# Kernel optimization log

Hardware: AMD Instinct MI355X
Metric: run time of the kernel (lower is better)

Reference implementation:

```python
import jax, jax.numpy as jnp
import numpy as np

B, S, D, H = 2, 2048, 1024, 16
DK = D // H  # 64
ROPE_THETA = 10000.0


def apply_rope(t, positions):
    # t: [B, H, S, DK]; positions: [B, S]
    half = DK // 2
    inv_freq = 1.0 / (ROPE_THETA ** (jnp.arange(0, DK, 2, dtype=jnp.float32) / DK))  # [half]
    ang = positions.astype(jnp.float32)[:, None, :, None] * inv_freq  # [B,1,S,half]
    cos, sin = jnp.cos(ang), jnp.sin(ang)
    t_even = t[..., 0::2]
    t_odd = t[..., 1::2]
    r_even = t_even * cos - t_odd * sin
    r_odd = t_even * sin + t_odd * cos
    # interleave back to original layout
    return jnp.stack([r_even, r_odd], axis=-1).reshape(t.shape)


def setup_inputs() -> dict:
    key = jax.random.key(0)
    ks = jax.random.split(key, 5)
    x = jax.random.normal(ks[0], (B, S, D), dtype=jnp.float32)
    token_positions = jnp.broadcast_to(jnp.arange(S, dtype=jnp.int64 if jax.config.jax_enable_x64 else jnp.int32), (B, S))
    w_q = jax.random.normal(ks[1], (D, D), dtype=jnp.float32)
    w_k = jax.random.normal(ks[2], (D, D), dtype=jnp.float32)
    w_v = jax.random.normal(ks[3], (D, D), dtype=jnp.float32)
    w_o = jax.random.normal(ks[4], (D, D), dtype=jnp.float32)
    return {"x": x, "token_positions": token_positions, "w_q": w_q, "w_k": w_k, "w_v": w_v, "w_o": w_o}


def reference(x, token_positions, w_q, w_k, w_v, w_o):
    # project: weights stored as (h*d_k, d_model)
    wq = w_q.reshape(H, DK, D)
    wk = w_k.reshape(H, DK, D)
    wv = w_v.reshape(H, DK, D)
    q = jnp.einsum('bsd,hkd->bhsk', x, wq)  # [B,H,S,DK]
    k = jnp.einsum('bsd,hkd->bhsk', x, wk)
    v = jnp.einsum('bsd,hkd->bhsk', x, wv)
    q = apply_rope(q, token_positions)
    k = apply_rope(k, token_positions)
    scale = 1.0 / jnp.sqrt(jnp.float32(DK))
    scores = jnp.einsum('bhnk,bhmk->bhnm', q, k) * scale  # [B,H,S,S]
    causal = jnp.tril(jnp.ones((S, S), dtype=bool))
    scores = jnp.where(causal, scores, -jnp.inf)
    attn = jax.nn.softmax(scores, axis=-1)
    out = jnp.einsum('bhnm,bhmv->bhnv', attn, v)  # [B,H,S,DK]
    out = jnp.transpose(out, (0, 2, 1, 3)).reshape(B, S, H * DK)
    return jnp.einsum('bsf,df->bsd', out, w_o)
```

## Files before the change

### kernel.cpp

```cpp
#include <hip/hip_runtime.h>

typedef unsigned short u16;
typedef unsigned int u32;
typedef __attribute__((ext_vector_type(8))) __bf16 bf16x8;
typedef __attribute__((ext_vector_type(4))) float f32x4;

#define NSEQ 2048
#define NDIM 1024
#define NHEAD 16
#define NTOK 4096
#define NX   4194304
#define NWEL 1048576

__device__ __forceinline__ u16 f2bf(float f) {
  unsigned u = __float_as_uint(f);
  return (u16)((u + 0x7fffu + ((u >> 16) & 1u)) >> 16);
}
__device__ __forceinline__ float bf2f(u16 h) {
  return __uint_as_float(((unsigned)h) << 16);
}
__device__ __forceinline__ bf16x8 ld16(const u16* p) {
  int4 v = *reinterpret_cast<const int4*>(p);
  return __builtin_bit_cast(bf16x8, v);
}
__device__ __forceinline__ f32x4 mfma16(bf16x8 a, bf16x8 b, f32x4 c) {
  return __builtin_amdgcn_mfma_f32_16x16x32_bf16(a, b, c, 0, 0, 0);
}
__device__ __forceinline__ u32 cvtpk(float lo, float hi) {
  u32 r;
  asm("v_cvt_pk_bf16_f32 %0, %1, %2" : "=v"(r) : "v"(lo), "v"(hi));
  return r;
}
__device__ __forceinline__ float max3f(float a, float b, float c) {
  float d;
  asm("v_max3_f32 %0, %1, %2, %3" : "=v"(d) : "v"(a), "v"(b), "v"(c));
  return d;
}
__device__ __forceinline__ void gload16(const u16* g, u16* l) {
  __builtin_amdgcn_global_load_lds(
      (const __attribute__((address_space(1))) void*)g,
      (__attribute__((address_space(3))) void*)l, 16, 0, 0);
}

#define GEMM_PROLOGUE                                                         \
  const int tid = threadIdx.x;                                                \
  const int lane = tid & 63, wid = tid >> 6;                                  \
  const int wm = wid >> 1, wn = wid & 1;                                      \
  const int lr = lane & 15, lg = lane >> 4;                                   \
  const int srow_ = tid >> 2;                                                 \
  const int sch_ = ((tid & 3) ^ ((tid >> 3) & 3)) * 8;                        \
  const int rsw_ = (lg ^ ((lr >> 1) & 3)) * 8;

#define STAGE3(BB, AH, AL, BH, BL, T0, J0, K0)                                \
  {                                                                           \
    u16* bb_ = (BB);                                                          \
    gload16(AH + (size_t)((T0) + srow_) * NDIM + (K0) + sch_, bb_ + tid * 8); \
    gload16(AH + (size_t)((T0) + 64 + srow_) * NDIM + (K0) + sch_,            \
            bb_ + 2048 + tid * 8);                                            \
    gload16(BH + (size_t)((J0) + srow_) * NDIM + (K0) + sch_,                 \
            bb_ + 4096 + tid * 8);                                            \
    gload16(BH + (size_t)((J0) + 64 + srow_) * NDIM + (K0) + sch_,            \
            bb_ + 6144 + tid * 8);                                            \
    gload16(AL + (size_t)((T0) + srow_) * NDIM + (K0) + sch_,                 \
            bb_ + 8192 + tid * 8);                                            \
    gload16(AL + (size_t)((T0) + 64 + srow_) * NDIM + (K0) + sch_,            \
            bb_ + 10240 + tid * 8);                                           \
    gload16(BL + (size_t)((J0) + srow_) * NDIM + (K0) + sch_,                 \
            bb_ + 12288 + tid * 8);                                           \
    gload16(BL + (size_t)((J0) + 64 + srow_) * NDIM + (K0) + sch_,            \
            bb_ + 14336 + tid * 8);                                           \
  }

#define GEMM3_LOOP(AH, AL, BH, BL, T0, J0)                                    \
  STAGE3(lds, AH, AL, BH, BL, T0, J0, 0)                                      \
  __syncthreads();                                                            \
  for (int k0 = 0; k0 < NDIM; k0 += 32) {                                     \
    u16* cb_ = lds + ((k0 >> 5) & 1) * 16384;                                 \
    if (k0 + 32 < NDIM) {                                                     \
      u16* nb_ = lds + ((((k0 >> 5) & 1) ^ 1) * 16384);                       \
      STAGE3(nb_, AH, AL, BH, BL, T0, J0, k0 + 32)                            \
    }                                                                         \
    bf16x8 afh[4], afl[4];                                                    \
    _Pragma("unroll") for (int m = 0; m < 4; m++) {                           \
      int off = (wm * 64 + m * 16 + lr) * 32 + rsw_;                          \
      afh[m] = ld16(cb_ + off);                                               \
      afl[m] = ld16(cb_ + 8192 + off);                                        \
    }                                                                         \
    _Pragma("unroll") for (int n = 0; n < 4; n++) {                           \
      int off = (wn * 64 + n * 16 + lr) * 32 + rsw_;                          \
      bf16x8 bfh = ld16(cb_ + 4096 + off);                                    \
      bf16x8 bfl = ld16(cb_ + 12288 + off);                                   \
      _Pragma("unroll") for (int m = 0; m < 4; m++) {                         \
        acc[m][n] = mfma16(afh[m], bfh, acc[m][n]);                           \
        acc[m][n] = mfma16(afh[m], bfl, acc[m][n]);                           \
        acc[m][n] = mfma16(afl[m], bfh, acc[m][n]);                           \
      }                                                                       \
    }                                                                         \
    __syncthreads();                                                          \
  }

#define STAGE1(BB, AH, BH, T0, J0, K0)                                        \
  {                                                                           \
    u16* bb_ = (BB);                                                          \
    gload16(AH + (size_t)((T0) + srow_) * NDIM + (K0) + sch_, bb_ + tid * 8); \
    gload16(AH + (size_t)((T0) + 64 + srow_) * NDIM + (K0) + sch_,            \
            bb_ + 2048 + tid * 8);                                            \
    gload16(BH + (size_t)((J0) + srow_) * NDIM + (K0) + sch_,                 \
            bb_ + 4096 + tid * 8);                                            \
    gload16(BH + (size_t)((J0) + 64 + srow_) * NDIM + (K0) + sch_,            \
            bb_ + 6144 + tid * 8);                                            \
  }

#define GEMM1_LOOP(AH, BH, T0, J0)                                            \
  STAGE1(lds, AH, BH, T0, J0, 0)                                              \
  __syncthreads();                                                            \
  for (int k0 = 0; k0 < NDIM; k0 += 32) {                                     \
    u16* cb_ = lds + ((k0 >> 5) & 1) * 8192;                                  \
    if (k0 + 32 < NDIM) {                                                     \
      u16* nb_ = lds + ((((k0 >> 5) & 1) ^ 1) * 8192);                        \
      STAGE1(nb_, AH, BH, T0, J0, k0 + 32)                                    \
    }                                                                         \
    bf16x8 afh[4];                                                            \
    _Pragma("unroll") for (int m = 0; m < 4; m++) {                           \
      int off = (wm * 64 + m * 16 + lr) * 32 + rsw_;                          \
      afh[m] = ld16(cb_ + off);                                               \
    }                                                                         \
    _Pragma("unroll") for (int n = 0; n < 4; n++) {                           \
      int off = (wn * 64 + n * 16 + lr) * 32 + rsw_;                          \
      bf16x8 bfh = ld16(cb_ + 4096 + off);                                    \
      _Pragma("unroll") for (int m = 0; m < 4; m++) {                         \
        acc[m][n] = mfma16(afh[m], bfh, acc[m][n]);                           \
      }                                                                       \
    }                                                                         \
    __syncthreads();                                                          \
  }

__global__ __launch_bounds__(256) void k_prep(
    const float* __restrict__ x, const float* __restrict__ wq,
    const float* __restrict__ wk, const float* __restrict__ wv,
    const float* __restrict__ wo,
    u16* __restrict__ xh, u16* __restrict__ xl,
    u16* __restrict__ wh, u16* __restrict__ wl) {
  int g = blockIdx.x * 256 + threadIdx.x;
  const float4* src;
  u16 *dh, *dl;
  int idx;
  bool wantlo = true;
  if (g < NX / 4) {
    src = (const float4*)x; dh = xh; dl = xl; idx = g;
  } else {
    int z = (g - NX / 4) / (NWEL / 4);
    int r = (g - NX / 4) % (NWEL / 4);
    src = (const float4*)(z == 0 ? wq : z == 1 ? wk : z == 2 ? wv : wo);
    dh = wh + (size_t)z * NWEL; dl = wl + (size_t)z * NWEL; idx = r;
    wantlo = (z < 2);
  }
  float4 v = src[idx];
  u16 h0 = f2bf(v.x), h1 = f2bf(v.y), h2 = f2bf(v.z), h3 = f2bf(v.w);
  ushort4 hv = make_ushort4(h0, h1, h2, h3);
  ((ushort4*)dh)[idx] = hv;
  if (wantlo) {
    ushort4 lv = make_ushort4(f2bf(v.x - bf2f(h0)), f2bf(v.y - bf2f(h1)),
                              f2bf(v.z - bf2f(h2)), f2bf(v.w - bf2f(h3)));
    ((ushort4*)dl)[idx] = lv;
  }
}

__global__ __launch_bounds__(256) void k_tab(float2* __restrict__ csn) {
  int idx = blockIdx.x * 256 + threadIdx.x;
  int p = idx >> 5, j = idx & 31;
  double invf = exp((double)(2 * j) * (-9.210340371976184 / 64.0));
  double ang = (double)p * invf;
  double kq = rint(ang * 0.15915494309189535);
  float a = (float)(ang - kq * 6.283185307179586);
  csn[idx] = make_float2(cosf(a), sinf(a));
}

__global__ __launch_bounds__(256) void k_qkv(
    const u16* __restrict__ xh, const u16* __restrict__ xl,
    const u16* __restrict__ wh, const u16* __restrict__ wl,
    const int* __restrict__ tokpos, const float2* __restrict__ csn,
    u16* __restrict__ qh, u16* __restrict__ ql,
    u16* __restrict__ kh, u16* __restrict__ kl) {
  __shared__ __align__(16) u16 lds[32768];
  const int z = blockIdx.z;
  const int t0 = blockIdx.y * 128, j0 = blockIdx.x * 128;
  const int h0 = j0 >> 6;
  GEMM_PROLOGUE
  const u16* Bh = wh + (size_t)z * NWEL;
  const u16* Bl = wl + (size_t)z * NWEL;
  f32x4 acc[4][4];
#pragma unroll
  for (int m = 0; m < 4; m++)
#pragma unroll
    for (int n = 0; n < 4; n++) acc[m][n] = f32x4{0.f, 0.f, 0.f, 0.f};
  GEMM3_LOOP(xh, xl, Bh, Bl, t0, j0)

  const int b = t0 >> 11, s0 = t0 & 2047;
  u16* dh = (z == 0) ? qh : kh;
  u16* dl = (z == 0) ? ql : kl;
  const float scl = (z == 0) ? 0.18033688011112042f : 1.0f;
#pragma unroll
  for (int m = 0; m < 4; m++) {
#pragma unroll
    for (int r = 0; r < 4; r++) {
      int pos = tokpos[t0 + wm * 64 + m * 16 + lg * 4 + r];
      int rloc = wm * 64 + m * 16 + lg * 4 + r;
#pragma unroll
      for (int n = 0; n < 4; n++) {
        float val = acc[m][n][r];
        float nb = __shfl_xor(val, 1);
        int dk = (wn * 64 + n * 16 + lr) & 63;
        float2 cs = csn[pos * 32 + (dk >> 1)];
        float v = ((dk & 1) ? (nb * cs.y + val * cs.x)
                            : (val * cs.x - nb * cs.y)) * scl;
        int cloc = wn * 64 + n * 16 + lr;
        u16 hi = f2bf(v);
        lds[rloc * 128 + cloc] = hi;
        lds[16384 + rloc * 128 + cloc] = f2bf(v - bf2f(hi));
      }
    }
  }
  __syncthreads();
#pragma unroll
  for (int i = 0; i < 16; i++) {
    int idx = tid + i * 256;
    int plane = idx >> 11, i2 = idx & 2047;
    int r = i2 >> 4, cc = i2 & 15;
    int4 v = *(int4*)(lds + plane * 16384 + r * 128 + cc * 8);
    int h2 = cc >> 3, dk = (cc & 7) * 8;
    u16* dst = plane ? dl : dh;
    size_t off = ((size_t)((b * NHEAD + h0 + h2) * NSEQ + s0 + r)) * 64 + dk;
    *(int4*)(dst + off) = v;
  }
}

__global__ __launch_bounds__(256) void k_v(
    const u16* __restrict__ xh, const u16* __restrict__ wvh,
    u16* __restrict__ vt) {
  __shared__ __align__(16) u16 lds[16384];
  const int t0 = blockIdx.y * 128, j0 = blockIdx.x * 128;
  const int h0 = j0 >> 6;
  GEMM_PROLOGUE
  f32x4 acc[4][4];
#pragma unroll
  for (int m = 0; m < 4; m++)
#pragma unroll
    for (int n = 0; n < 4; n++) acc[m][n] = f32x4{0.f, 0.f, 0.f, 0.f};
  GEMM1_LOOP(xh, wvh, t0, j0)
  const int b = t0 >> 11, s0 = t0 & 2047;
#pragma unroll
  for (int m = 0; m < 4; m++)
#pragma unroll
    for (int r = 0; r < 4; r++) {
      int rloc = wm * 64 + m * 16 + lg * 4 + r;
#pragma unroll
      for (int n = 0; n < 4; n++) {
        int cloc = wn * 64 + n * 16 + lr;
        lds[cloc * 128 + (rloc ^ ((cloc & 15) << 3))] = f2bf(acc[m][n][r]);
      }
    }
  __syncthreads();
#pragma unroll
  for (int i = 0; i < 8; i++) {
    int idx = tid + i * 256;
    int col = idx >> 4, rc = idx & 15;
    int4 v = *(int4*)(lds + col * 128 + ((rc * 8) ^ ((col & 15) << 3)));
    int h2 = col >> 6, dk = col & 63;
    size_t off = ((size_t)((b * NHEAD + h0 + h2) * 64 + dk)) * NSEQ + s0 + rc * 8;
    *(int4*)(vt + off) = v;
  }
}

#define ATT_STAGE(SEL)                                                        \
  _Pragma("unroll") for (int j_ = 0; j_ < 3; j_++) {                          \
    gload16(asrc[j_], adst[j_] + (SEL) * 4096);                               \
    asrc[j_] += astr[j_];                                                     \
  }

__global__ __launch_bounds__(512) void k_attn(
    const u16* __restrict__ qh, const u16* __restrict__ ql,
    const u16* __restrict__ kh, const u16* __restrict__ kl,
    const u16* __restrict__ vt, u16* __restrict__ ah) {
  __shared__ __align__(16) u16 skh[2][4096];
  __shared__ __align__(16) u16 skl[2][4096];
  __shared__ __align__(16) u16 svb[2][4096];
  __shared__ __align__(16) u16 sp[8192];
  const int tid = threadIdx.x, lane = tid & 63, w = tid >> 6;
  const int lr = lane & 15, lg = lane >> 4;
  const int wl4 = w & 3;
  const int fid = blockIdx.y * 16 + blockIdx.x;
  const int vb_ = (fid & 7) * 64 + (fid >> 3);
  const int bh = vb_ >> 4;
  const int qpair = vb_ & 15;
  const size_t base = (size_t)bh * NSEQ * 64;
  const size_t vbase = (size_t)bh * 64 * NSEQ;
  const int b = bh >> 4, h = bh & 15;
  const int qbA = 31 - qpair;
  const int myq = (w < 4) ? qbA : qpair;
  const int q0 = myq * 64;
  const int ntA = qbA + 1;

  const int qrow_g = q0 + wl4 * 16 + lr;
  bf16x8 qfh[2], qfl[2];
#pragma unroll
  for (int kk = 0; kk < 2; kk++) {
    qfh[kk] = ld16(qh + base + (size_t)qrow_g * 64 + kk * 32 + lg * 8);
    qfl[kk] = ld16(ql + base + (size_t)qrow_g * 64 + kk * 32 + lg * 8);
  }
  float mrun = -__builtin_inff(), lrun = 0.f;
  f32x4 oacc[4];
#pragma unroll
  for (int nf = 0; nf < 4; nf++) oacc[nf] = f32x4{0.f, 0.f, 0.f, 0.f};

  const u16* asrc[3];
  u16* adst[3];
  int astr[3];
#pragma unroll
  for (int j_ = 0; j_ < 3; j_++) {
    int seg_ = w * 3 + j_;
    int ten_ = seg_ >> 3, sub_ = seg_ & 7;
    int row_ = sub_ * 8 + (lane >> 3);
    int sc_ = ((lane & 7) * 8) ^ ((row_ & 7) * 8);
    adst[j_] = (ten_ == 0 ? &skh[0][0] : ten_ == 1 ? &skl[0][0] : &svb[0][0]) +
               sub_ * 512;
    astr[j_] = (ten_ == 2) ? 64 : 4096;
    asrc[j_] = (ten_ == 2)
                   ? vt + vbase + (size_t)row_ * NSEQ + sc_
                   : (ten_ == 0 ? kh : kl) + base + (size_t)row_ * 64 + sc_;
  }

  int sel = 0;
  ATT_STAGE(0)
  __syncthreads();
  for (int kt = 0; kt < ntA; kt++) {
    if (kt + 1 < ntA) { ATT_STAGE(sel ^ 1) }
    if (kt <= myq) {
      f32x4 sacc[4];
#pragma unroll
      for (int nf = 0; nf < 4; nf++) sacc[nf] = f32x4{0.f, 0.f, 0.f, 0.f};
      __builtin_amdgcn_s_setprio(1);
#pragma unroll
      for (int nf = 0; nf < 4; nf++) {
        int krow = nf * 16 + lr;
        int swz = (krow & 7) * 8;
#pragma unroll
        for (int kk = 0; kk < 2; kk++) {
          int off = krow * 64 + ((kk * 32 + lg * 8) ^ swz);
          bf16x8 kfh = ld16(&skh[sel][0] + off);
          bf16x8 kfl = ld16(&skl[sel][0] + off);
          sacc[nf] = mfma16(kfh, qfh[kk], sacc[nf]);
          sacc[nf] = mfma16(kfl, qfh[kk], sacc[nf]);
          sacc[nf] = mfma16(kfh, qfl[kk], sacc[nf]);
        }
      }
      __builtin_amdgcn_s_setprio(0);
      float sv[4][4], mm[4];
#pragma unroll
      for (int nf = 0; nf < 4; nf++) {
#pragma unroll
        for (int r = 0; r < 4; r++) sv[nf][r] = sacc[nf][r];
      }
      if (kt == myq) {
#pragma unroll
        for (int nf = 0; nf < 4; nf++)
#pragma unroll
          for (int r = 0; r < 4; r++) {
            int colg = kt * 64 + nf * 16 + lg * 4 + r;
            if (colg > qrow_g) sv[nf][r] = -__builtin_inff();
          }
      }
#pragma unroll
      for (int nf = 0; nf < 4; nf++)
        mm[nf] = fmaxf(max3f(sv[nf][0], sv[nf][1], sv[nf][2]), sv[nf][3]);
      float rmax = fmaxf(max3f(mm[0], mm[1], mm[2]), mm[3]);
      rmax = fmaxf(rmax, __shfl_xor(rmax, 16));
      rmax = fmaxf(rmax, __shfl_xor(rmax, 32));
      float alpha = 1.f;
      bool resc = __any(rmax > mrun + 8.f);
      if (resc) {
        float mnew = fmaxf(mrun, rmax);
        alpha = exp2f(mrun - mnew);
        mrun = mnew;
        lrun *= alpha;
      }
      float p[4][4];
      float ss[4];
#pragma unroll
      for (int nf = 0; nf < 4; nf++) {
#pragma unroll
        for (int r = 0; r < 4; r++) p[nf][r] = exp2f(sv[nf][r] - mrun);
        ss[nf] = (p[nf][0] + p[nf][1]) + (p[nf][2] + p[nf][3]);
      }
      float rsum = (ss[0] + ss[1]) + (ss[2] + ss[3]);
      rsum += __shfl_xor(rsum, 16);
      rsum += __shfl_xor(rsum, 32);
      lrun += rsum;
      {
        int prow = w * 16 + lr;
        int swz = (prow & 7) * 8;
#pragma unroll
        for (int nf = 0; nf < 4; nf++) {
          u32 w0 = cvtpk(p[nf][0], p[nf][1]);
          u32 w1 = cvtpk(p[nf][2], p[nf][3]);
          int col = (nf * 16 + lg * 4) ^ swz;
          *(uint2*)(&sp[prow * 64 + col]) = make_uint2(w0, w1);
        }
      }
      if (resc) {
        float af0 = __shfl(alpha, lg * 4 + 0);
        float af1 = __shfl(alpha, lg * 4 + 1);
        float af2 = __shfl(alpha, lg * 4 + 2);
        float af3 = __shfl(alpha, lg * 4 + 3);
#pragma unroll
        for (int nf = 0; nf < 4; nf++) {
          oacc[nf][0] *= af0; oacc[nf][1] *= af1;
          oacc[nf][2] *= af2; oacc[nf][3] *= af3;
        }
      }
      {
        int prow = w * 16 + lr;
        int pswz = (prow & 7) * 8;
        __builtin_amdgcn_s_setprio(1);
#pragma unroll
        for (int kk = 0; kk < 2; kk++) {
          bf16x8 pa = ld16(&sp[prow * 64 + ((kk * 32 + lg * 8) ^ pswz)]);
#pragma unroll
          for (int nf = 0; nf < 4; nf++) {
            int vrow = nf * 16 + lr;
            bf16x8 vb2 = ld16(&svb[sel][0] + vrow * 64 +
                              ((kk * 32 + lg * 8) ^ ((vrow & 7) * 8)));
            oacc[nf] = mfma16(pa, vb2, oacc[nf]);
          }
        }
        __builtin_amdgcn_s_setprio(0);
      }
    }
    __syncthreads();
    sel ^= 1;
  }
  float inv = 1.0f / lrun;
  float iv0 = __shfl(inv, lg * 4 + 0);
  float iv1 = __shfl(inv, lg * 4 + 1);
  float iv2 = __shfl(inv, lg * 4 + 2);
  float iv3 = __shfl(inv, lg * 4 + 3);
#pragma unroll
  for (int r = 0; r < 4; r++) {
    float ivr = r == 0 ? iv0 : r == 1 ? iv1 : r == 2 ? iv2 : iv3;
    int row = q0 + wl4 * 16 + lg * 4 + r;
    size_t toff = ((size_t)(b * NSEQ + row)) * NDIM + h * 64;
#pragma unroll
    for (int nf = 0; nf < 4; nf++) {
      ah[toff + nf * 16 + lr] = f2bf(oacc[nf][r] * ivr);
    }
  }
}

__global__ __launch_bounds__(256) void k_out(
    const u16* __restrict__ ah, const u16* __restrict__ wh,
    float* __restrict__ out) {
  __shared__ __align__(16) u16 lds[16384];
  const int t0 = blockIdx.y * 128, j0 = blockIdx.x * 128;
  GEMM_PROLOGUE
  f32x4 acc[4][4];
#pragma unroll
  for (int m = 0; m < 4; m++)
#pragma unroll
    for (int n = 0; n < 4; n++) acc[m][n] = f32x4{0.f, 0.f, 0.f, 0.f};
  GEMM1_LOOP(ah, wh, t0, j0)
#pragma unroll
  for (int m = 0; m < 4; m++)
#pragma unroll
    for (int r = 0; r < 4; r++) {
      int row = t0 + wm * 64 + m * 16 + lg * 4 + r;
#pragma unroll
      for (int n = 0; n < 4; n++) {
        int col = j0 + wn * 64 + n * 16 + lr;
        out[(size_t)row * NDIM + col] = acc[m][n][r];
      }
    }
}

extern "C" void kernel_launch(void* const* d_in, const int* in_sizes, int n_in,
                              void* d_out, int out_size, void* d_ws, size_t ws_size,
                              hipStream_t stream) {
  (void)in_sizes; (void)n_in; (void)out_size; (void)ws_size;
  const float* x = (const float*)d_in[0];
  const int* tokpos = (const int*)d_in[1];
  const float* wq = (const float*)d_in[2];
  const float* wk = (const float*)d_in[3];
  const float* wv = (const float*)d_in[4];
  const float* wo = (const float*)d_in[5];
  float* out = (float*)d_out;

  u16* ws = (u16*)d_ws;
  u16* xh = ws;
  u16* xl = xh + NX;
  u16* wh = xl + NX;
  u16* wl = wh + 4 * (size_t)NWEL;
  u16* qh = wl + 4 * (size_t)NWEL;
  u16* ql = qh + NX;
  u16* kh = ql + NX;
  u16* kl = kh + NX;
  u16* vt = kl + NX;
  float2* csn = (float2*)(vt + NX);

  k_prep<<<dim3(8192), dim3(256), 0, stream>>>(x, wq, wk, wv, wo, xh, xl, wh, wl);
  k_tab<<<dim3(256), dim3(256), 0, stream>>>(csn);
  k_qkv<<<dim3(8, 32, 2), dim3(256), 0, stream>>>(xh, xl, wh, wl, tokpos, csn,
                                                  qh, ql, kh, kl);
  k_v<<<dim3(8, 32), dim3(256), 0, stream>>>(xh, wh + 2 * (size_t)NWEL, vt);
  k_attn<<<dim3(16, 32), dim3(512), 0, stream>>>(qh, ql, kh, kl, vt, xh);
  k_out<<<dim3(8, 32), dim3(256), 0, stream>>>(xh, wh + 3 * (size_t)NWEL, out);
}
```

Measured before the change: 173.5 us.

## Enlarge QKV GEMM tile to 256 rows and use triple-buffered async loads

The Q/K projection kernel now runs 512 threads per block over a 256x128 output tile, which halves the grid. Its K-loop is pipelined with three LDS stages, explicit vmcnt waits and raw barriers, so global-to-LDS loads run two steps ahead of the MFMA work. Incremented pointers replace per-stage address recomputation. The goal is to cut weight reloads and barrier stalls, at the cost of much more LDS per block (144KB), which may limit occupancy to one block per CU.

New measurement: 178.2 us. 1.03x slower.

```diff
diff --git a/kernel.cpp b/kernel.cpp
--- a/kernel.cpp
+++ b/kernel.cpp
@@ -50,54 +50,6 @@
   const int srow_ = tid >> 2;                                                 \
   const int sch_ = ((tid & 3) ^ ((tid >> 3) & 3)) * 8;                        \
   const int rsw_ = (lg ^ ((lr >> 1) & 3)) * 8;
-
-#define STAGE3(BB, AH, AL, BH, BL, T0, J0, K0)                                \
-  {                                                                           \
-    u16* bb_ = (BB);                                                          \
-    gload16(AH + (size_t)((T0) + srow_) * NDIM + (K0) + sch_, bb_ + tid * 8); \
-    gload16(AH + (size_t)((T0) + 64 + srow_) * NDIM + (K0) + sch_,            \
-            bb_ + 2048 + tid * 8);                                            \
-    gload16(BH + (size_t)((J0) + srow_) * NDIM + (K0) + sch_,                 \
-            bb_ + 4096 + tid * 8);                                            \
-    gload16(BH + (size_t)((J0) + 64 + srow_) * NDIM + (K0) + sch_,            \
-            bb_ + 6144 + tid * 8);                                            \
-    gload16(AL + (size_t)((T0) + srow_) * NDIM + (K0) + sch_,                 \
-            bb_ + 8192 + tid * 8);                                            \
-    gload16(AL + (size_t)((T0) + 64 + srow_) * NDIM + (K0) + sch_,            \
-            bb_ + 10240 + tid * 8);                                           \
-    gload16(BL + (size_t)((J0) + srow_) * NDIM + (K0) + sch_,                 \
-            bb_ + 12288 + tid * 8);                                           \
-    gload16(BL + (size_t)((J0) + 64 + srow_) * NDIM + (K0) + sch_,            \
-            bb_ + 14336 + tid * 8);                                           \
-  }
-
-#define GEMM3_LOOP(AH, AL, BH, BL, T0, J0)                                    \
-  STAGE3(lds, AH, AL, BH, BL, T0, J0, 0)                                      \
-  __syncthreads();                                                            \
-  for (int k0 = 0; k0 < NDIM; k0 += 32) {                                     \
-    u16* cb_ = lds + ((k0 >> 5) & 1) * 16384;                                 \
-    if (k0 + 32 < NDIM) {                                                     \
-      u16* nb_ = lds + ((((k0 >> 5) & 1) ^ 1) * 16384);                       \
-      STAGE3(nb_, AH, AL, BH, BL, T0, J0, k0 + 32)                            \
-    }                                                                         \
-    bf16x8 afh[4], afl[4];                                                    \
-    _Pragma("unroll") for (int m = 0; m < 4; m++) {                           \
-      int off = (wm * 64 + m * 16 + lr) * 32 + rsw_;                          \
-      afh[m] = ld16(cb_ + off);                                               \
-      afl[m] = ld16(cb_ + 8192 + off);                                        \
-    }                                                                         \
-    _Pragma("unroll") for (int n = 0; n < 4; n++) {                           \
-      int off = (wn * 64 + n * 16 + lr) * 32 + rsw_;                          \
-      bf16x8 bfh = ld16(cb_ + 4096 + off);                                    \
-      bf16x8 bfl = ld16(cb_ + 12288 + off);                                   \
-      _Pragma("unroll") for (int m = 0; m < 4; m++) {                         \
-        acc[m][n] = mfma16(afh[m], bfh, acc[m][n]);                           \
-        acc[m][n] = mfma16(afh[m], bfl, acc[m][n]);                           \
-        acc[m][n] = mfma16(afl[m], bfh, acc[m][n]);                           \
-      }                                                                       \
-    }                                                                         \
-    __syncthreads();                                                          \
-  }
 
 #define STAGE1(BB, AH, BH, T0, J0, K0)                                        \
   {                                                                           \
@@ -176,25 +128,88 @@
   csn[idx] = make_float2(cosf(a), sinf(a));
 }
 
-__global__ __launch_bounds__(256) void k_qkv(
+#define QSTAGE(BI)                                                            \
+  {                                                                           \
+    u16* bb_ = lds + (BI) * 24576;                                            \
+    gload16(p0, bb_ + tid * 8);                                               \
+    gload16(p1, bb_ + 4096 + tid * 8);                                        \
+    gload16(p2, bb_ + 8192 + tid * 8);                                        \
+    gload16(p3, bb_ + 12288 + tid * 8);                                       \
+    gload16(p4, bb_ + 16384 + tid * 8);                                       \
+    gload16(p5, bb_ + 20480 + tid * 8);                                       \
+    p0 += 32; p1 += 32; p2 += 32; p3 += 32; p4 += 32; p5 += 32;               \
+  }
+
+__global__ __launch_bounds__(512) void k_qkv(
     const u16* __restrict__ xh, const u16* __restrict__ xl,
     const u16* __restrict__ wh, const u16* __restrict__ wl,
     const int* __restrict__ tokpos, const float2* __restrict__ csn,
     u16* __restrict__ qh, u16* __restrict__ ql,
     u16* __restrict__ kh, u16* __restrict__ kl) {
-  __shared__ __align__(16) u16 lds[32768];
+  __shared__ __align__(16) u16 lds[73728];
   const int z = blockIdx.z;
-  const int t0 = blockIdx.y * 128, j0 = blockIdx.x * 128;
+  const int t0 = blockIdx.y * 256, j0 = blockIdx.x * 128;
   const int h0 = j0 >> 6;
-  GEMM_PROLOGUE
+  const int tid = threadIdx.x;
+  const int lane = tid & 63, wid = tid >> 6;
+  const int wm = wid >> 1, wn = wid & 1;
+  const int lr = lane & 15, lg = lane >> 4;
+  const int srow_ = tid >> 2;
+  const int sch_ = ((tid & 3) ^ ((tid >> 3) & 3)) * 8;
+  const int rsw_ = (lg ^ ((lr >> 1) & 3)) * 8;
   const u16* Bh = wh + (size_t)z * NWEL;
   const u16* Bl = wl + (size_t)z * NWEL;
+
+  const u16* p0 = xh + (size_t)(t0 + srow_) * NDIM + sch_;
+  const u16* p1 = xh + (size_t)(t0 + 128 + srow_) * NDIM + sch_;
+  const u16* p2 = Bh + (size_t)(j0 + srow_) * NDIM + sch_;
+  const u16* p3 = xl + (size_t)(t0 + srow_) * NDIM + sch_;
+  const u16* p4 = xl + (size_t)(t0 + 128 + srow_) * NDIM + sch_;
+  const u16* p5 = Bl + (size_t)(j0 + srow_) * NDIM + sch_;
+
   f32x4 acc[4][4];
 #pragma unroll
   for (int m = 0; m < 4; m++)
 #pragma unroll
     for (int n = 0; n < 4; n++) acc[m][n] = f32x4{0.f, 0.f, 0.f, 0.f};
-  GEMM3_LOOP(xh, xl, Bh, Bl, t0, j0)
+
+  int cur = 0, stg = 2;
+  QSTAGE(0)
+  QSTAGE(1)
+  for (int it = 0; it < 32; it++) {
+    if (it < 31)
+      asm volatile("s_waitcnt vmcnt(6)" ::: "memory");
+    else
+      asm volatile("s_waitcnt vmcnt(0)" ::: "memory");
+    __builtin_amdgcn_s_barrier();
+    asm volatile("" ::: "memory");
+    if (it + 2 < 32) {
+      QSTAGE(stg)
+      stg = (stg == 2) ? 0 : stg + 1;
+    }
+    u16* cb_ = lds + cur * 24576;
+    bf16x8 afh[4], afl[4];
+#pragma unroll
+    for (int m = 0; m < 4; m++) {
+      int off = (wm * 64 + m * 16 + lr) * 32 + rsw_;
+      afh[m] = ld16(cb_ + off);
+      afl[m] = ld16(cb_ + 12288 + off);
+    }
+#pragma unroll
+    for (int n = 0; n < 4; n++) {
+      int off = (wn * 64 + n * 16 + lr) * 32 + rsw_;
+      bf16x8 bfh = ld16(cb_ + 8192 + off);
+      bf16x8 bfl = ld16(cb_ + 20480 + off);
+#pragma unroll
+      for (int m = 0; m < 4; m++) {
+        acc[m][n] = mfma16(afh[m], bfh, acc[m][n]);
+        acc[m][n] = mfma16(afh[m], bfl, acc[m][n]);
+        acc[m][n] = mfma16(afl[m], bfh, acc[m][n]);
+      }
+    }
+    cur = (cur == 2) ? 0 : cur + 1;
+  }
+  __syncthreads();
 
   const int b = t0 >> 11, s0 = t0 & 2047;
   u16* dh = (z == 0) ? qh : kh;
@@ -217,17 +232,17 @@
         int cloc = wn * 64 + n * 16 + lr;
         u16 hi = f2bf(v);
         lds[rloc * 128 + cloc] = hi;
-        lds[16384 + rloc * 128 + cloc] = f2bf(v - bf2f(hi));
+        lds[32768 + rloc * 128 + cloc] = f2bf(v - bf2f(hi));
       }
     }
   }
   __syncthreads();
 #pragma unroll
   for (int i = 0; i < 16; i++) {
-    int idx = tid + i * 256;
-    int plane = idx >> 11, i2 = idx & 2047;
+    int idx = tid + i * 512;
+    int plane = idx >> 12, i2 = idx & 4095;
     int r = i2 >> 4, cc = i2 & 15;
-    int4 v = *(int4*)(lds + plane * 16384 + r * 128 + cc * 8);
+    int4 v = *(int4*)(lds + plane * 32768 + r * 128 + cc * 8);
     int h2 = cc >> 3, dk = (cc & 7) * 8;
     u16* dst = plane ? dl : dh;
     size_t off = ((size_t)((b * NHEAD + h0 + h2) * NSEQ + s0 + r)) * 64 + dk;
@@ -507,7 +522,7 @@
 
   k_prep<<<dim3(8192), dim3(256), 0, stream>>>(x, wq, wk, wv, wo, xh, xl, wh, wl);
   k_tab<<<dim3(256), dim3(256), 0, stream>>>(csn);
-  k_qkv<<<dim3(8, 32, 2), dim3(256), 0, stream>>>(xh, xl, wh, wl, tokpos, csn,
+  k_qkv<<<dim3(8, 16, 2), dim3(512), 0, stream>>>(xh, xl, wh, wl, tokpos, csn,
                                                   qh, ql, kh, kl);
   k_v<<<dim3(8, 32), dim3(256), 0, stream>>>(xh, wh + 2 * (size_t)NWEL, vt);
   k_attn<<<dim3(16, 32), dim3(512), 0, stream>>>(qh, ql, kh, kl, vt, xh);
```
